# Kernel tuning notes

Hardware: AMD Instinct MI355X
Metric: run time of the kernel (lower is better)

## Reference

```python
import jax, jax.numpy as jnp
import numpy as np

B, N, FIN, H, F = 8, 1024, 256, 8, 64
NEG_SLOPE = 0.2


def setup_inputs() -> dict:
    key = jax.random.key(0)
    k = jax.random.split(key, 6)
    x = jax.random.normal(k[0], (B, N, FIN), dtype=jnp.float32)
    adj_mask = jax.random.randint(k[1], (B, N, N), 0, 2, dtype=jnp.int32)
    edge_prior = jax.random.normal(k[2], (B, N, N), dtype=jnp.float32)
    # params (xavier-style scales)
    W = jax.random.normal(k[3], (FIN, H * F), dtype=jnp.float32) * np.sqrt(2.0 / (FIN + H * F))
    a_left = jax.random.normal(k[4], (H, F), dtype=jnp.float32) * np.sqrt(2.0 / (1 + F))
    a_right = jax.random.normal(k[5], (H, F), dtype=jnp.float32) * np.sqrt(2.0 / (1 + F))
    edge_scale = jnp.float32(0.05)
    return {"x": x, "adj_mask": adj_mask, "edge_prior": edge_prior,
            "W": W, "a_left": a_left, "a_right": a_right, "edge_scale": edge_scale}


def reference(x, adj_mask, edge_prior, W, a_left, a_right, edge_scale):
    b, n, _ = x.shape
    h = (x @ W).reshape(b, n, H, F)                      # [B,N,H,F]
    e_left = jnp.einsum('bnhf,hf->bnh', h, a_left)       # [B,N,H]
    e_right = jnp.einsum('bnhf,hf->bnh', h, a_right)     # [B,N,H]
    e = jax.nn.leaky_relu(e_left[:, :, None, :] + e_right[:, None, :, :],
                          negative_slope=NEG_SLOPE)      # [B,N,N,H]
    e = e + edge_scale * edge_prior[..., None]
    e = jnp.where((adj_mask == 0)[..., None], -jnp.inf, e)
    alpha = jax.nn.softmax(e, axis=2)                    # softmax over neighbors j
    h_new = jnp.einsum('bijh,bjhf->bihf', alpha, h)      # [B,N,H,F]
    return h_new.reshape(b, n, H * F)                    # concat=True
```

## Files before the change

### kernel.cpp

```cpp
#include <hip/hip_runtime.h>
#include <hip/hip_bf16.h>

#define B_ 8
#define N_ 1024
#define FIN_ 256
#define H_ 8
#define F_ 64
#define HF_ 512
#define BN_ 8192
#define LOG2E 1.4426950408889634f

using bf16x8 = __attribute__((ext_vector_type(8))) short;
using f32x4  = __attribute__((ext_vector_type(4))) float;
using i32x4  = __attribute__((ext_vector_type(4))) int;

__device__ __forceinline__ short f2bf(float x) {
  __hip_bfloat16 b = __float2bfloat16(x);
  return *reinterpret_cast<short*>(&b);
}
__device__ __forceinline__ float bf2f(short s) {
  union { unsigned u; float f; } v;
  v.u = ((unsigned)(unsigned short)s) << 16;
  return v.f;
}

__global__ __launch_bounds__(256) void k_cvt(
    const float* __restrict__ x, const float* __restrict__ W,
    short* __restrict__ xb, short* __restrict__ Wt) {
  const int bid = blockIdx.x;
  if (bid < 1024) {
    const int idx = (bid * 256 + threadIdx.x) * 8;
    f32x4 a = *(const f32x4*)(x + idx);
    f32x4 b = *(const f32x4*)(x + idx + 4);
    bf16x8 o;
    o[0]=f2bf(a[0]); o[1]=f2bf(a[1]); o[2]=f2bf(a[2]); o[3]=f2bf(a[3]);
    o[4]=f2bf(b[0]); o[5]=f2bf(b[1]); o[6]=f2bf(b[2]); o[7]=f2bf(b[3]);
    *(bf16x8*)(xb + idx) = o;
  } else {
    const int idx = (bid - 1024) * 256 + threadIdx.x;
    const int f = idx >> 8, c = idx & 255;
    Wt[f * FIN_ + c] = f2bf(W[c * HF_ + f]);
  }
}

__global__ __launch_bounds__(256) void k_pre(
    const float* __restrict__ prior, const int* __restrict__ mask,
    const float* __restrict__ esp, short* __restrict__ cmat) {
  const float es = esp[0] * LOG2E;
  const size_t idx = ((size_t)blockIdx.x * 256 + threadIdx.x) * 8;
  f32x4 p0 = *(const f32x4*)(prior + idx);
  f32x4 p1 = *(const f32x4*)(prior + idx + 4);
  i32x4 m0 = *(const i32x4*)(mask + idx);
  i32x4 m1 = *(const i32x4*)(mask + idx + 4);
  bf16x8 o;
#pragma unroll
  for (int e = 0; e < 4; e++) {
    o[e]     = f2bf(m0[e] != 0 ? es * p0[e] : -1e30f);
    o[e + 4] = f2bf(m1[e] != 0 ? es * p1[e] : -1e30f);
  }
  *(bf16x8*)(cmat + idx) = o;
}

__global__ __launch_bounds__(256) void k_h(
    const short* __restrict__ Wt, const short* __restrict__ xb,
    const float* __restrict__ aL, const float* __restrict__ aR,
    short* __restrict__ h_t, float* __restrict__ el_t, float* __restrict__ er_t) {
  const int nt = blockIdx.x;
  const int h  = blockIdx.y;
  const int w  = threadIdx.x >> 6;
  const int l  = threadIdx.x & 63;
  const int lr = l & 15, lk = l >> 4;
  const int n0 = nt * 64;
  const int fbase = h * 64 + w * 16;

  f32x4 acc[4] = {};
  const short* arow = Wt + (fbase + lr) * FIN_ + lk * 8;

#pragma unroll
  for (int k0 = 0; k0 < FIN_; k0 += 32) {
    bf16x8 a = *(const bf16x8*)(arow + k0);
#pragma unroll
    for (int nf = 0; nf < 4; nf++) {
      bf16x8 bb = *(const bf16x8*)(xb + (size_t)(n0 + nf * 16 + lr) * FIN_ + k0 + lk * 8);
      acc[nf] = __builtin_amdgcn_mfma_f32_16x16x32_bf16(a, bb, acc[nf], 0, 0, 0);
    }
  }

  __shared__ float sEl[4][64], sEr[4][64];
  float al[4], ar[4];
#pragma unroll
  for (int r = 0; r < 4; r++) {
    const int fl = w * 16 + lk * 4 + r;
    al[r] = aL[h * F_ + fl];
    ar[r] = aR[h * F_ + fl];
  }
#pragma unroll
  for (int nf = 0; nf < 4; nf++) {
    const int n = n0 + nf * 16 + lr;
#pragma unroll
    for (int r = 0; r < 4; r++)
      h_t[(size_t)(fbase + lk * 4 + r) * BN_ + n] = f2bf(acc[nf][r]);
    float pl = acc[nf][0]*al[0] + acc[nf][1]*al[1] + acc[nf][2]*al[2] + acc[nf][3]*al[3];
    float pr = acc[nf][0]*ar[0] + acc[nf][1]*ar[1] + acc[nf][2]*ar[2] + acc[nf][3]*ar[3];
    pl += __shfl_xor(pl, 16); pl += __shfl_xor(pl, 32);
    pr += __shfl_xor(pr, 16); pr += __shfl_xor(pr, 32);
    if (lk == 0) { sEl[w][nf * 16 + lr] = pl; sEr[w][nf * 16 + lr] = pr; }
  }
  __syncthreads();
  if (threadIdx.x < 64) {
    const int n = threadIdx.x;
    el_t[h * BN_ + n0 + n] = (sEl[0][n] + sEl[1][n] + sEl[2][n] + sEl[3][n]) * LOG2E;
    er_t[h * BN_ + n0 + n] = (sEr[0][n] + sEr[1][n] + sEr[2][n] + sEr[3][n]) * LOG2E;
  }
}

__global__ __launch_bounds__(256) void k_rep(
    const short* __restrict__ h_t, short* __restrict__ hA) {
  const size_t T = (size_t)blockIdx.x * 256 + threadIdx.x;
  const int l  = T & 63;
  const int ff = (T >> 6) & 3;
  const int js = (T >> 8) & 31;
  const int bh = (int)(T >> 13);
  const int b = bh >> 3, h = bh & 7;
  const int f = h * 64 + ff * 16 + (l & 15);
  const int col = b * 1024 + js * 32 + (l >> 4) * 8;
  bf16x8 v = *(const bf16x8*)(h_t + (size_t)f * BN_ + col);
  *(bf16x8*)(hA + T * 8) = v;
}

__global__ __launch_bounds__(512, 4) void k_attn(
    const short* __restrict__ hA, const float* __restrict__ el_t,
    const float* __restrict__ er_t, const short* __restrict__ cmat,
    float* __restrict__ out) {
  const int b  = blockIdx.x >> 6;
  const int it = blockIdx.x & 63;
  const int t  = threadIdx.x;
  const int h  = t >> 6;
  const int l  = t & 63;
  const int lr = l & 15, lk = l >> 4;
  const int i0 = it * 16;
  const size_t bn = (size_t)b * N_;

  __shared__ short cbuf[2][4096];

  const float el = el_t[h * BN_ + bn + i0 + lr];
  const float* erp = er_t + h * BN_ + bn + lk * 8;
  const short* hW  = hA + (size_t)(b * 8 + h) * 65536 + l * 8;
  const int rr = t >> 5, sl = t & 31;
  const short* cg = cmat + (bn + i0 + rr) * (size_t)N_ + ((sl ^ (rr & 7)) * 8);

  bf16x8 stg0 = *(const bf16x8*)(cg);
  *(bf16x8*)(&cbuf[0][0] + t * 8) = stg0;
  bf16x8 hN[4];
#pragma unroll
  for (int ff = 0; ff < 4; ff++) hN[ff] = *(const bf16x8*)(hW + ff * 512);
  __syncthreads();

  f32x4 acc[4] = {};
  f32x4 accS = {};
  bf16x8 ones;
#pragma unroll
  for (int e = 0; e < 8; e++) ones[e] = (short)0x3F80;

  for (int ch = 0; ch < 4; ++ch) {
    bf16x8 stgN;
    if (ch < 3) stgN = *(const bf16x8*)(cg + (ch + 1) * 256);
    const short* cb = &cbuf[ch & 1][0];
#pragma unroll
    for (int js = 0; js < 8; ++js) {
      const int s = ch * 8 + js;
      bf16x8 h0 = hN[0], h1 = hN[1], h2 = hN[2], h3 = hN[3];
      const int sn = (s < 31) ? s + 1 : 31;
      const short* hs = hW + (size_t)sn * 2048;
      hN[0] = *(const bf16x8*)(hs);
      hN[1] = *(const bf16x8*)(hs + 512);
      hN[2] = *(const bf16x8*)(hs + 1024);
      hN[3] = *(const bf16x8*)(hs + 1536);
      f32x4 er0 = *(const f32x4*)(erp + s * 32);
      f32x4 er1 = *(const f32x4*)(erp + s * 32 + 4);
      bf16x8 cf = *(const bf16x8*)(cb + lr * 256 + (((js * 4 + lk) ^ (lr & 7)) * 8));
      float pe[8];
#pragma unroll
      for (int q = 0; q < 4; q++) {
        float sA = el + er0[q];
        sA = fmaxf(sA, 0.2f * sA);
        sA += bf2f(cf[q]);
        asm("v_exp_f32 %0, %1" : "=v"(pe[q]) : "v"(sA));
        float sB = el + er1[q];
        sB = fmaxf(sB, 0.2f * sB);
        sB += bf2f(cf[q + 4]);
        asm("v_exp_f32 %0, %1" : "=v"(pe[q + 4]) : "v"(sB));
      }
      bf16x8 pf;
#pragma unroll
      for (int e = 0; e < 8; e++) pf[e] = f2bf(pe[e]);
      accS   = __builtin_amdgcn_mfma_f32_16x16x32_bf16(ones, pf, accS, 0, 0, 0);
      acc[0] = __builtin_amdgcn_mfma_f32_16x16x32_bf16(h0, pf, acc[0], 0, 0, 0);
      acc[1] = __builtin_amdgcn_mfma_f32_16x16x32_bf16(h1, pf, acc[1], 0, 0, 0);
      acc[2] = __builtin_amdgcn_mfma_f32_16x16x32_bf16(h2, pf, acc[2], 0, 0, 0);
      acc[3] = __builtin_amdgcn_mfma_f32_16x16x32_bf16(h3, pf, acc[3], 0, 0, 0);
    }
    if (ch < 3) {
      __syncthreads();
      *(bf16x8*)(&cbuf[(ch + 1) & 1][0] + t * 8) = stgN;
      __syncthreads();
    }
  }

  const float inv = 1.0f / accS[0];
  const size_t row = bn + i0 + lr;
#pragma unroll
  for (int ff = 0; ff < 4; ff++) {
    f32x4 v = acc[ff];
    v[0] *= inv; v[1] *= inv; v[2] *= inv; v[3] *= inv;
    *(f32x4*)(out + row * HF_ + h * 64 + ff * 16 + lk * 4) = v;
  }
}

extern "C" void kernel_launch(void* const* d_in, const int* in_sizes, int n_in,
                              void* d_out, int out_size, void* d_ws, size_t ws_size,
                              hipStream_t stream) {
  const float* x     = (const float*)d_in[0];
  const int*   adj   = (const int*)  d_in[1];
  const float* prior = (const float*)d_in[2];
  const float* W     = (const float*)d_in[3];
  const float* aL    = (const float*)d_in[4];
  const float* aR    = (const float*)d_in[5];
  const float* es    = (const float*)d_in[6];
  float* out = (float*)d_out;

  char* ws = (char*)d_ws;
  short* h_t  = (short*)ws;
  short* hA   = (short*)(ws + 8u  * 1024 * 1024);
  short* xb   = (short*)(ws + 16u * 1024 * 1024);
  short* Wt   = (short*)(ws + 20u * 1024 * 1024);
  float* el_t = (float*)(ws + 20u * 1024 * 1024 + 262144);
  float* er_t = (float*)(ws + 20u * 1024 * 1024 + 524288);
  short* cmat = (short*)(ws + 21u * 1024 * 1024);

  hipLaunchKernelGGL(k_cvt, dim3(1536), dim3(256), 0, stream, x, W, xb, Wt);
  hipLaunchKernelGGL(k_pre, dim3(4096), dim3(256), 0, stream, prior, adj, es, cmat);
  hipLaunchKernelGGL(k_h,   dim3(128, 8), dim3(256), 0, stream,
                     Wt, xb, aL, aR, h_t, el_t, er_t);
  hipLaunchKernelGGL(k_rep, dim3(2048), dim3(256), 0, stream, h_t, hA);
  hipLaunchKernelGGL(k_attn, dim3(512), dim3(512), 0, stream,
                     hA, el_t, er_t, cmat, out);
}
```

Measured before the change: 79.22 us.

## Fuse mask/prior preprocessing and h repacking into attention and projection kernels

Removes the standalone k_pre pass so k_attn reads the fp32 prior and int mask directly and converts them into the swizzled LDS tile. This avoids writing and rereading the bf16 cmat buffer. Removes k_rep by transposing the h tile through shared memory in k_h and writing the MFMA-ready hA layout directly. k_attn now processes 32 query rows per block (two MFMA row groups sharing each h operand) with 256 blocks, which lowers occupancy and raises register use in exchange for reuse of h loads.

```diff
diff --git a/kernel.cpp b/kernel.cpp
--- a/kernel.cpp
+++ b/kernel.cpp
@@ -9,6 +9,7 @@
 #define HF_ 512
 #define BN_ 8192
 #define LOG2E 1.4426950408889634f
+#define NEG_ 0.2f
 
 using bf16x8 = __attribute__((ext_vector_type(8))) short;
 using f32x4  = __attribute__((ext_vector_type(4))) float;
@@ -22,6 +23,15 @@
   union { unsigned u; float f; } v;
   v.u = ((unsigned)(unsigned short)s) << 16;
   return v.f;
+}
+__device__ __forceinline__ bf16x8 cvtCE(f32x4 pa, f32x4 pb, i32x4 ma, i32x4 mb, float es) {
+  bf16x8 o;
+#pragma unroll
+  for (int e = 0; e < 4; e++) {
+    o[e]     = f2bf(ma[e] != 0 ? es * pa[e] : -1e30f);
+    o[e + 4] = f2bf(mb[e] != 0 ? es * pb[e] : -1e30f);
+  }
+  return o;
 }
 
 __global__ __launch_bounds__(256) void k_cvt(
@@ -43,28 +53,10 @@
   }
 }
 
-__global__ __launch_bounds__(256) void k_pre(
-    const float* __restrict__ prior, const int* __restrict__ mask,
-    const float* __restrict__ esp, short* __restrict__ cmat) {
-  const float es = esp[0] * LOG2E;
-  const size_t idx = ((size_t)blockIdx.x * 256 + threadIdx.x) * 8;
-  f32x4 p0 = *(const f32x4*)(prior + idx);
-  f32x4 p1 = *(const f32x4*)(prior + idx + 4);
-  i32x4 m0 = *(const i32x4*)(mask + idx);
-  i32x4 m1 = *(const i32x4*)(mask + idx + 4);
-  bf16x8 o;
-#pragma unroll
-  for (int e = 0; e < 4; e++) {
-    o[e]     = f2bf(m0[e] != 0 ? es * p0[e] : -1e30f);
-    o[e + 4] = f2bf(m1[e] != 0 ? es * p1[e] : -1e30f);
-  }
-  *(bf16x8*)(cmat + idx) = o;
-}
-
 __global__ __launch_bounds__(256) void k_h(
     const short* __restrict__ Wt, const short* __restrict__ xb,
     const float* __restrict__ aL, const float* __restrict__ aR,
-    short* __restrict__ h_t, float* __restrict__ el_t, float* __restrict__ er_t) {
+    short* __restrict__ hA, float* __restrict__ el_t, float* __restrict__ er_t) {
   const int nt = blockIdx.x;
   const int h  = blockIdx.y;
   const int w  = threadIdx.x >> 6;
@@ -86,6 +78,7 @@
     }
   }
 
+  __shared__ short sT[64][72];
   __shared__ float sEl[4][64], sEr[4][64];
   float al[4], ar[4];
 #pragma unroll
@@ -96,15 +89,15 @@
   }
 #pragma unroll
   for (int nf = 0; nf < 4; nf++) {
-    const int n = n0 + nf * 16 + lr;
+    const int nl = nf * 16 + lr;
 #pragma unroll
     for (int r = 0; r < 4; r++)
-      h_t[(size_t)(fbase + lk * 4 + r) * BN_ + n] = f2bf(acc[nf][r]);
+      sT[w * 16 + lk * 4 + r][nl] = f2bf(acc[nf][r]);
     float pl = acc[nf][0]*al[0] + acc[nf][1]*al[1] + acc[nf][2]*al[2] + acc[nf][3]*al[3];
     float pr = acc[nf][0]*ar[0] + acc[nf][1]*ar[1] + acc[nf][2]*ar[2] + acc[nf][3]*ar[3];
     pl += __shfl_xor(pl, 16); pl += __shfl_xor(pl, 32);
     pr += __shfl_xor(pr, 16); pr += __shfl_xor(pr, 32);
-    if (lk == 0) { sEl[w][nf * 16 + lr] = pl; sEr[w][nf * 16 + lr] = pr; }
+    if (lk == 0) { sEl[w][nl] = pl; sEr[w][nl] = pr; }
   }
   __syncthreads();
   if (threadIdx.x < 64) {
@@ -112,60 +105,80 @@
     el_t[h * BN_ + n0 + n] = (sEl[0][n] + sEl[1][n] + sEl[2][n] + sEl[3][n]) * LOG2E;
     er_t[h * BN_ + n0 + n] = (sEr[0][n] + sEr[1][n] + sEr[2][n] + sEr[3][n]) * LOG2E;
   }
-}
-
-__global__ __launch_bounds__(256) void k_rep(
-    const short* __restrict__ h_t, short* __restrict__ hA) {
-  const size_t T = (size_t)blockIdx.x * 256 + threadIdx.x;
-  const int l  = T & 63;
-  const int ff = (T >> 6) & 3;
-  const int js = (T >> 8) & 31;
-  const int bh = (int)(T >> 13);
-  const int b = bh >> 3, h = bh & 7;
-  const int f = h * 64 + ff * 16 + (l & 15);
-  const int col = b * 1024 + js * 32 + (l >> 4) * 8;
-  bf16x8 v = *(const bf16x8*)(h_t + (size_t)f * BN_ + col);
-  *(bf16x8*)(hA + T * 8) = v;
-}
-
-__global__ __launch_bounds__(512, 4) void k_attn(
+  const int b8h = (nt >> 4) * 8 + h;
+  const int jb  = (nt & 15) * 2;
+#pragma unroll
+  for (int gi = 0; gi < 2; gi++) {
+    const int g   = threadIdx.x * 2 + gi;
+    const int jsl = g >> 8, ff = (g >> 6) & 3, gl = g & 63;
+    const int glr = gl & 15, glk = gl >> 4;
+    bf16x8 v = *(const bf16x8*)(&sT[ff * 16 + glr][jsl * 32 + glk * 8]);
+    *(bf16x8*)(hA + (((size_t)b8h * 32 + jb + jsl) * 4 + ff) * 512 + gl * 8) = v;
+  }
+}
+
+__global__ __launch_bounds__(512, 2) void k_attn(
     const short* __restrict__ hA, const float* __restrict__ el_t,
-    const float* __restrict__ er_t, const short* __restrict__ cmat,
+    const float* __restrict__ er_t, const float* __restrict__ prior,
+    const int* __restrict__ mask, const float* __restrict__ esp,
     float* __restrict__ out) {
-  const int b  = blockIdx.x >> 6;
-  const int it = blockIdx.x & 63;
+  const int bid = blockIdx.x;
+  const int b  = bid & 7;
+  const int it = bid >> 3;
   const int t  = threadIdx.x;
   const int h  = t >> 6;
   const int l  = t & 63;
   const int lr = l & 15, lk = l >> 4;
-  const int i0 = it * 16;
+  const int i0 = it * 32;
   const size_t bn = (size_t)b * N_;
-
-  __shared__ short cbuf[2][4096];
-
-  const float el = el_t[h * BN_ + bn + i0 + lr];
+  const float es = esp[0] * LOG2E;
+
+  __shared__ short cbuf[2][8192];
+
+  const float* elh = el_t + h * BN_ + bn + i0;
+  const float el0 = elh[lr], el1 = elh[16 + lr];
   const float* erp = er_t + h * BN_ + bn + lk * 8;
   const short* hW  = hA + (size_t)(b * 8 + h) * 65536 + l * 8;
-  const int rr = t >> 5, sl = t & 31;
-  const short* cg = cmat + (bn + i0 + rr) * (size_t)N_ + ((sl ^ (rr & 7)) * 8);
-
-  bf16x8 stg0 = *(const bf16x8*)(cg);
-  *(bf16x8*)(&cbuf[0][0] + t * 8) = stg0;
+
+  const int srow = t >> 4;
+  const int c0   = (t & 15) * 2;
+  const int sw   = srow & 7;
+  const int gA   = (c0 ^ sw) & ~1;
+  const int slotA = (srow * 32 + (gA ^ sw)) * 8;
+  const int slotB = (srow * 32 + ((gA | 1) ^ sw)) * 8;
+  const size_t grow = (bn + i0 + srow) * (size_t)N_;
+  const float* pg = prior + grow + gA * 8;
+  const int*   mg = mask  + grow + gA * 8;
+
+  {
+    f32x4 p0 = *(const f32x4*)(pg),     p1 = *(const f32x4*)(pg + 4);
+    f32x4 p2 = *(const f32x4*)(pg + 8), p3 = *(const f32x4*)(pg + 12);
+    i32x4 m0 = *(const i32x4*)(mg),     m1 = *(const i32x4*)(mg + 4);
+    i32x4 m2 = *(const i32x4*)(mg + 8), m3 = *(const i32x4*)(mg + 12);
+    *(bf16x8*)(&cbuf[0][slotA]) = cvtCE(p0, p1, m0, m1, es);
+    *(bf16x8*)(&cbuf[0][slotB]) = cvtCE(p2, p3, m2, m3, es);
+  }
   bf16x8 hN[4];
 #pragma unroll
   for (int ff = 0; ff < 4; ff++) hN[ff] = *(const bf16x8*)(hW + ff * 512);
   __syncthreads();
 
-  f32x4 acc[4] = {};
-  f32x4 accS = {};
+  f32x4 acc[4][2] = {};
+  f32x4 accS[2] = {};
   bf16x8 ones;
 #pragma unroll
   for (int e = 0; e < 8; e++) ones[e] = (short)0x3F80;
 
   for (int ch = 0; ch < 4; ++ch) {
-    bf16x8 stgN;
-    if (ch < 3) stgN = *(const bf16x8*)(cg + (ch + 1) * 256);
-    const short* cb = &cbuf[ch & 1][0];
+    f32x4 p0, p1, p2, p3; i32x4 m0, m1, m2, m3;
+    if (ch < 3) {
+      const int off = (ch + 1) * 256;
+      p0 = *(const f32x4*)(pg + off);      p1 = *(const f32x4*)(pg + off + 4);
+      p2 = *(const f32x4*)(pg + off + 8);  p3 = *(const f32x4*)(pg + off + 12);
+      m0 = *(const i32x4*)(mg + off);      m1 = *(const i32x4*)(mg + off + 4);
+      m2 = *(const i32x4*)(mg + off + 8);  m3 = *(const i32x4*)(mg + off + 12);
+    }
+    const short* cb = cbuf[ch & 1];
 #pragma unroll
     for (int js = 0; js < 8; ++js) {
       const int s = ch * 8 + js;
@@ -178,42 +191,54 @@
       hN[3] = *(const bf16x8*)(hs + 1536);
       f32x4 er0 = *(const f32x4*)(erp + s * 32);
       f32x4 er1 = *(const f32x4*)(erp + s * 32 + 4);
-      bf16x8 cf = *(const bf16x8*)(cb + lr * 256 + (((js * 4 + lk) ^ (lr & 7)) * 8));
-      float pe[8];
+      const int ci = ((js * 4 + lk) ^ (lr & 7)) * 8;
+      bf16x8 cA = *(const bf16x8*)(cb + lr * 256 + ci);
+      bf16x8 cB = *(const bf16x8*)(cb + (16 + lr) * 256 + ci);
+      bf16x8 pfA, pfB;
 #pragma unroll
       for (int q = 0; q < 4; q++) {
-        float sA = el + er0[q];
-        sA = fmaxf(sA, 0.2f * sA);
-        sA += bf2f(cf[q]);
-        asm("v_exp_f32 %0, %1" : "=v"(pe[q]) : "v"(sA));
-        float sB = el + er1[q];
-        sB = fmaxf(sB, 0.2f * sB);
-        sB += bf2f(cf[q + 4]);
-        asm("v_exp_f32 %0, %1" : "=v"(pe[q + 4]) : "v"(sB));
+        const float e0 = er0[q], e1 = er1[q];
+        float a1 = el0 + e0; a1 = fmaxf(a1, NEG_ * a1); a1 += bf2f(cA[q]);
+        float a2 = el0 + e1; a2 = fmaxf(a2, NEG_ * a2); a2 += bf2f(cA[q + 4]);
+        float b1 = el1 + e0; b1 = fmaxf(b1, NEG_ * b1); b1 += bf2f(cB[q]);
+        float b2 = el1 + e1; b2 = fmaxf(b2, NEG_ * b2); b2 += bf2f(cB[q + 4]);
+        float x1, x2, x3, x4;
+        asm("v_exp_f32 %0, %1" : "=v"(x1) : "v"(a1));
+        asm("v_exp_f32 %0, %1" : "=v"(x2) : "v"(a2));
+        asm("v_exp_f32 %0, %1" : "=v"(x3) : "v"(b1));
+        asm("v_exp_f32 %0, %1" : "=v"(x4) : "v"(b2));
+        pfA[q] = f2bf(x1); pfA[q + 4] = f2bf(x2);
+        pfB[q] = f2bf(x3); pfB[q + 4] = f2bf(x4);
       }
-      bf16x8 pf;
-#pragma unroll
-      for (int e = 0; e < 8; e++) pf[e] = f2bf(pe[e]);
-      accS   = __builtin_amdgcn_mfma_f32_16x16x32_bf16(ones, pf, accS, 0, 0, 0);
-      acc[0] = __builtin_amdgcn_mfma_f32_16x16x32_bf16(h0, pf, acc[0], 0, 0, 0);
-      acc[1] = __builtin_amdgcn_mfma_f32_16x16x32_bf16(h1, pf, acc[1], 0, 0, 0);
-      acc[2] = __builtin_amdgcn_mfma_f32_16x16x32_bf16(h2, pf, acc[2], 0, 0, 0);
-      acc[3] = __builtin_amdgcn_mfma_f32_16x16x32_bf16(h3, pf, acc[3], 0, 0, 0);
+      accS[0]   = __builtin_amdgcn_mfma_f32_16x16x32_bf16(ones, pfA, accS[0], 0, 0, 0);
+      accS[1]   = __builtin_amdgcn_mfma_f32_16x16x32_bf16(ones, pfB, accS[1], 0, 0, 0);
+      acc[0][0] = __builtin_amdgcn_mfma_f32_16x16x32_bf16(h0, pfA, acc[0][0], 0, 0, 0);
+      acc[0][1] = __builtin_amdgcn_mfma_f32_16x16x32_bf16(h0, pfB, acc[0][1], 0, 0, 0);
+      acc[1][0] = __builtin_amdgcn_mfma_f32_16x16x32_bf16(h1, pfA, acc[1][0], 0, 0, 0);
+      acc[1][1] = __builtin_amdgcn_mfma_f32_16x16x32_bf16(h1, pfB, acc[1][1], 0, 0, 0);
+      acc[2][0] = __builtin_amdgcn_mfma_f32_16x16x32_bf16(h2, pfA, acc[2][0], 0, 0, 0);
+      acc[2][1] = __builtin_amdgcn_mfma_f32_16x16x32_bf16(h2, pfB, acc[2][1], 0, 0, 0);
+      acc[3][0] = __builtin_amdgcn_mfma_f32_16x16x32_bf16(h3, pfA, acc[3][0], 0, 0, 0);
+      acc[3][1] = __builtin_amdgcn_mfma_f32_16x16x32_bf16(h3, pfB, acc[3][1], 0, 0, 0);
     }
     if (ch < 3) {
+      short* nb = (short*)cbuf[(ch + 1) & 1];
+      *(bf16x8*)(nb + slotA) = cvtCE(p0, p1, m0, m1, es);
+      *(bf16x8*)(nb + slotB) = cvtCE(p2, p3, m2, m3, es);
       __syncthreads();
-      *(bf16x8*)(&cbuf[(ch + 1) & 1][0] + t * 8) = stgN;
-      __syncthreads();
-    }
-  }
-
-  const float inv = 1.0f / accS[0];
-  const size_t row = bn + i0 + lr;
-#pragma unroll
-  for (int ff = 0; ff < 4; ff++) {
-    f32x4 v = acc[ff];
-    v[0] *= inv; v[1] *= inv; v[2] *= inv; v[3] *= inv;
-    *(f32x4*)(out + row * HF_ + h * 64 + ff * 16 + lk * 4) = v;
+    }
+  }
+
+#pragma unroll
+  for (int fi = 0; fi < 2; fi++) {
+    const float inv = 1.0f / accS[fi][0];
+    const size_t row = bn + i0 + fi * 16 + lr;
+#pragma unroll
+    for (int ff = 0; ff < 4; ff++) {
+      f32x4 v = acc[ff][fi];
+      v[0] *= inv; v[1] *= inv; v[2] *= inv; v[3] *= inv;
+      *(f32x4*)(out + row * HF_ + h * 64 + ff * 16 + lk * 4) = v;
+    }
   }
 }
 
@@ -230,19 +255,15 @@
   float* out = (float*)d_out;
 
   char* ws = (char*)d_ws;
-  short* h_t  = (short*)ws;
-  short* hA   = (short*)(ws + 8u  * 1024 * 1024);
-  short* xb   = (short*)(ws + 16u * 1024 * 1024);
-  short* Wt   = (short*)(ws + 20u * 1024 * 1024);
-  float* el_t = (float*)(ws + 20u * 1024 * 1024 + 262144);
-  float* er_t = (float*)(ws + 20u * 1024 * 1024 + 524288);
-  short* cmat = (short*)(ws + 21u * 1024 * 1024);
+  short* hA   = (short*)ws;
+  short* xb   = (short*)(ws + 8u  * 1024 * 1024);
+  short* Wt   = (short*)(ws + 12u * 1024 * 1024);
+  float* el_t = (float*)(ws + 12u * 1024 * 1024 + 262144);
+  float* er_t = (float*)(ws + 12u * 1024 * 1024 + 524288);
 
   hipLaunchKernelGGL(k_cvt, dim3(1536), dim3(256), 0, stream, x, W, xb, Wt);
-  hipLaunchKernelGGL(k_pre, dim3(4096), dim3(256), 0, stream, prior, adj, es, cmat);
   hipLaunchKernelGGL(k_h,   dim3(128, 8), dim3(256), 0, stream,
-                     Wt, xb, aL, aR, h_t, el_t, er_t);
-  hipLaunchKernelGGL(k_rep, dim3(2048), dim3(256), 0, stream, h_t, hA);
-  hipLaunchKernelGGL(k_attn, dim3(512), dim3(512), 0, stream,
-                     hA, el_t, er_t, cmat, out);
-}
+                     Wt, xb, aL, aR, hA, el_t, er_t);
+  hipLaunchKernelGGL(k_attn, dim3(256), dim3(512), 0, stream,
+                     hA, el_t, er_t, prior, adj, es, out);
+}
```

Measured after the change: 75.40 us. 4.8% less time.
